# Performance work log

Measured on AMD Instinct MI355X. Metric: run time of the kernel, lower is better.

Reference implementation:

```python
import jax, jax.numpy as jnp
import numpy as np

N_KERNELS = 5
MUL_FACTOR = 2.0


def setup_inputs() -> dict:
    key = jax.random.key(0)
    k1, k2 = jax.random.split(key)
    X = jax.random.normal(k1, (4096, 512), dtype=jnp.float32)
    Y = jax.random.normal(k2, (4096, 512), dtype=jnp.float32)
    return {"X": X, "Y": Y}


def _mmd(X, Y):
    # multipliers: 2.0 ** (arange(5) - 2) = [0.25, 0.5, 1, 2, 4]
    mults = MUL_FACTOR ** (jnp.arange(N_KERNELS, dtype=jnp.float32) - N_KERNELS // 2)
    Z = jnp.concatenate([X, Y], axis=0)            # [N+M, D]
    n = Z.shape[0]
    # squared euclidean pairwise distances (cdist ** 2)
    sq = jnp.sum(Z * Z, axis=-1)                    # [N+M]
    D2 = sq[:, None] + sq[None, :] - 2.0 * (Z @ Z.T)
    D2 = jnp.maximum(D2, 0.0)                       # [N+M, N+M]
    # bandwidth from detached distances: sum / (n^2 - n)
    bw = jax.lax.stop_gradient(jnp.sum(D2)) / (n * n - n)
    # multi-bandwidth RBF sum over kernels
    K = jnp.sum(jnp.exp(-D2[None, :, :] / (bw * mults)[:, None, None]), axis=0)
    Nx = X.shape[0]
    XX = jnp.mean(K[:Nx, :Nx])
    XY = jnp.mean(K[:Nx, Nx:])
    YY = jnp.mean(K[Nx:, Nx:])
    return XX - 2.0 * XY + YY


def reference(X, Y):
    return _mmd(X, Y)
```

## Files before the change

kernel.cpp:

```cpp
#include <hip/hip_runtime.h>

#define N_ROWS 8192
#define NX     4096
#define DIM    512
#define BT     128
#define NT     64
#define BK     32

typedef __bf16 bf16_t;
typedef bf16_t bf16x8 __attribute__((ext_vector_type(8)));
typedef bf16_t bf16x4 __attribute__((ext_vector_type(4)));
typedef float  f32x4  __attribute__((ext_vector_type(4)));

#if __has_builtin(__builtin_amdgcn_exp2f)
  #define EXP2F __builtin_amdgcn_exp2f
#else
  #define EXP2F exp2f
#endif


__device__ __forceinline__ const float* zrow(const float* X, const float* Y, int r) {
    return (r < NX) ? (X + (size_t)r * DIM) : (Y + (size_t)(r - NX) * DIM);
}

__device__ __forceinline__ void gload_lds16(const bf16_t* g, bf16_t* l) {
    __builtin_amdgcn_global_load_lds(
        (__attribute__((address_space(1))) void*)(void*)(g),
        (__attribute__((address_space(3))) void*)(void*)(l), 16, 0, 0);
}

__global__ void k_prep(const float* __restrict__ X, const float* __restrict__ Y,
                       bf16_t* __restrict__ Zh, float* __restrict__ sqrow,
                       float* __restrict__ colsum) {
    int t = threadIdx.x;
    if (blockIdx.x == 0) { colsum[t] = 0.f; colsum[t + 256] = 0.f; }
    int wv = t >> 6, lane = t & 63;
    int row = blockIdx.x * 4 + wv;
    const float4* z4 = (const float4*)zrow(X, Y, row);
    float4 a = z4[lane], b = z4[lane + 64];
    bf16x4 ha = {(bf16_t)a.x, (bf16_t)a.y, (bf16_t)a.z, (bf16_t)a.w};
    bf16x4 hb = {(bf16_t)b.x, (bf16_t)b.y, (bf16_t)b.z, (bf16_t)b.w};
    *(bf16x4*)(Zh + (size_t)row * DIM + lane * 4) = ha;
    *(bf16x4*)(Zh + (size_t)row * DIM + 256 + lane * 4) = hb;
    float s = a.x*a.x + a.y*a.y + a.z*a.z + a.w*a.w
            + b.x*b.x + b.y*b.y + b.z*b.z + b.w*b.w;
    #pragma unroll
    for (int off = 32; off > 0; off >>= 1) s += __shfl_down(s, off);
    if (lane == 0) sqrow[row] = s;
}

__global__ void k_colsum(const float* X, const float* Y, float* colsum) {
    int c = threadIdx.x * 2;
    int r0 = blockIdx.x * 128;
    float s0 = 0.f, s1 = 0.f;
    for (int r = r0; r < r0 + 128; ++r) {
        const float* zr = zrow(X, Y, r);
        float2 v = *(const float2*)(zr + c);
        s0 += v.x; s1 += v.y;
    }
    atomicAdd(&colsum[c], s0);
    atomicAdd(&colsum[c + 1], s1);
}

__global__ void k_bw(const float* sqrow, const float* colsum, float* cvals, double* acc) {
    __shared__ double red[256];
    int t = threadIdx.x;
    double s1 = 0.0;
    for (int i = t; i < N_ROWS; i += 256) s1 += (double)sqrow[i];
    double cs = 0.0;
    for (int d = t; d < DIM; d += 256) { double v = colsum[d]; cs += v * v; }
    red[t] = s1; __syncthreads();
    for (int off = 128; off > 0; off >>= 1) { if (t < off) red[t] += red[t + off]; __syncthreads(); }
    double S1 = red[0]; __syncthreads();
    red[t] = cs; __syncthreads();
    for (int off = 128; off > 0; off >>= 1) { if (t < off) red[t] += red[t + off]; __syncthreads(); }
    if (t == 0) {
        double CS = red[0];
        double n = (double)N_ROWS;
        double sumD2 = 2.0 * n * S1 - 2.0 * CS;
        double bw = sumD2 / (n * n - n);
        const double LOG2E = 1.4426950408889634;
        double mult = 0.25;
        for (int k = 0; k < 5; ++k) {
            cvals[k] = (float)(-LOG2E / (bw * mult));
            mult *= 2.0;
        }
        *acc = 0.0;
    }
}

__global__ __launch_bounds__(256) void k_pair(const bf16_t* __restrict__ Zh,
                                              const float* __restrict__ sqrow,
                                              const float* __restrict__ cvals,
                                              double* acc) {
    int ti = blockIdx.x, tj = blockIdx.y;
    if (tj < ti) return;
    __shared__ bf16_t As[4096];
    __shared__ bf16_t Bs[4096];
    __shared__ float wsum[4];

    int t = threadIdx.x, lane = t & 63, wv = t >> 6;
    int wr = wv >> 1, wc = wv & 1;

    const bf16_t* gA[2]; const bf16_t* gB[2];
    bf16_t* ldsA[2]; bf16_t* ldsB[2];
    #pragma unroll
    for (int h = 0; h < 2; ++h) {
        int c = h * 256 + t;
        int r = c >> 2, sq = c & 3;
        int q = sq ^ ((r >> 1) & 3);
        gA[h] = Zh + (size_t)(ti * BT + r) * DIM + q * 8;
        gB[h] = Zh + (size_t)(tj * BT + r) * DIM + q * 8;
        int base = (h * 256 + wv * 64) * 8;
        ldsA[h] = As + base;
        ldsB[h] = Bs + base;
    }

    int n16 = lane & 15, q16 = lane >> 4;
    int aoff[4], boff[4];
    #pragma unroll
    for (int aa = 0; aa < 4; ++aa) {
        int r = 16 * (wr * 4 + aa) + n16;
        aoff[aa] = (r * 4 + (q16 ^ ((r >> 1) & 3))) * 8;
    }
    #pragma unroll
    for (int bb = 0; bb < 4; ++bb) {
        int r = 16 * (wc * 4 + bb) + n16;
        boff[bb] = (r * 4 + (q16 ^ ((r >> 1) & 3))) * 8;
    }

    f32x4 accf[4][4];
    #pragma unroll
    for (int a = 0; a < 4; ++a)
        #pragma unroll
        for (int b = 0; b < 4; ++b)
            accf[a][b] = (f32x4){0.f, 0.f, 0.f, 0.f};

    for (int kt = 0; kt < DIM; kt += BK) {
        if (kt) __syncthreads();
        #pragma unroll
        for (int h = 0; h < 2; ++h) {
            gload_lds16(gA[h] + kt, ldsA[h]);
            gload_lds16(gB[h] + kt, ldsB[h]);
        }
        __syncthreads();
        bf16x8 a[4], b[4];
        #pragma unroll
        for (int aa = 0; aa < 4; ++aa) a[aa] = *(const bf16x8*)(As + aoff[aa]);
        #pragma unroll
        for (int bb = 0; bb < 4; ++bb) b[bb] = *(const bf16x8*)(Bs + boff[bb]);
        #pragma unroll
        for (int aa = 0; aa < 4; ++aa)
            #pragma unroll
            for (int bb = 0; bb < 4; ++bb)
                accf[aa][bb] = __builtin_amdgcn_mfma_f32_16x16x32_bf16(
                    a[aa], b[bb], accf[aa][bb], 0, 0, 0);
    }

    float c4 = cvals[4];
    int i0 = ti * BT + wr * 64;
    int j0 = tj * BT + wc * 64;

    float sqi[4][4], sqj[4];
    #pragma unroll
    for (int aa = 0; aa < 4; ++aa)
        #pragma unroll
        for (int r = 0; r < 4; ++r)
            sqi[aa][r] = sqrow[i0 + 16 * aa + q16 * 4 + r];
    #pragma unroll
    for (int bb = 0; bb < 4; ++bb)
        sqj[bb] = sqrow[j0 + 16 * bb + n16];

    float s_local = 0.f;
    #pragma unroll
    for (int aa = 0; aa < 4; ++aa) {
        #pragma unroll
        for (int bb = 0; bb < 4; ++bb) {
            #pragma unroll
            for (int r = 0; r < 4; ++r) {
                float d2 = fmaf(-2.f, accf[aa][bb][r], sqi[aa][r] + sqj[bb]);
                d2 = fmaxf(d2, 0.f);
                float e4 = EXP2F(d2 * c4);
                float e3 = e4 * e4;
                float e2 = e3 * e3;
                float e1 = e2 * e2;
                float e0 = e1 * e1;
                s_local += e4 + e3 + e2 + e1 + e0;
            }
        }
    }
    #pragma unroll
    for (int off = 32; off > 0; off >>= 1) s_local += __shfl_down(s_local, off);
    if (lane == 0) wsum[wv] = s_local;
    __syncthreads();
    if (t == 0) {
        float bs = wsum[0] + wsum[1] + wsum[2] + wsum[3];
        double si = (ti < NT / 2) ? 1.0 : -1.0;
        double sj = (tj < NT / 2) ? 1.0 : -1.0;
        double w = si * sj * ((ti == tj) ? 1.0 : 2.0);
        atomicAdd(acc, w * (double)bs);
    }
}

__global__ void k_final(const double* acc, float* out) {
    out[0] = (float)(*acc / ((double)NX * (double)NX));
}

extern "C" void kernel_launch(void* const* d_in, const int* in_sizes, int n_in,
                              void* d_out, int out_size, void* d_ws, size_t ws_size,
                              hipStream_t stream) {
    const float* X = (const float*)d_in[0];
    const float* Y = (const float*)d_in[1];
    float* out = (float*)d_out;

    float*  sqrow  = (float*)d_ws;
    float*  colsum = sqrow + 8192;
    float*  cvals  = (float*)((char*)d_ws + 34816);
    double* acc    = (double*)((char*)d_ws + 34840);
    bf16_t* Zh     = (bf16_t*)((char*)d_ws + 36864);

    k_prep  <<<2048, 256, 0, stream>>>(X, Y, Zh, sqrow, colsum);
    k_colsum<<<64, 256, 0, stream>>>(X, Y, colsum);
    k_bw    <<<1, 256, 0, stream>>>(sqrow, colsum, cvals, acc);
    k_pair  <<<dim3(NT, NT), 256, 0, stream>>>(Zh, sqrow, cvals, acc);
    k_final <<<1, 1, 0, stream>>>(acc, out);
}
```

Baseline: 152.8 us.

## Pre-swizzle bf16 Z into MFMA fragment layout and drop LDS staging

The prep kernel now writes the bf16 copy of Z in an MFMA-fragment-ready layout, so the pair kernel loads its A/B operands straight from global memory into registers with a one-step prefetch. This removes the LDS staging and the per-k-step barriers. The column-sum kernel is merged into prep, and the final division moves into the pair kernel through a last-block counter, which saves two launches. The cost is that operand reuse now relies on L2/L1 caching instead of LDS sharing across waves, and extra register pressure comes from the prefetch buffers.

```diff
diff --git a/kernel.cpp b/kernel.cpp
--- a/kernel.cpp
+++ b/kernel.cpp
@@ -5,11 +5,12 @@
 #define DIM    512
 #define BT     128
 #define NT     64
-#define BK     32
+#define NB     (NT * (NT + 1) / 2)
+#define NGRP   512
+#define NCH    16
 
 typedef __bf16 bf16_t;
 typedef bf16_t bf16x8 __attribute__((ext_vector_type(8)));
-typedef bf16_t bf16x4 __attribute__((ext_vector_type(4)));
 typedef float  f32x4  __attribute__((ext_vector_type(4)));
 
 #if __has_builtin(__builtin_amdgcn_exp2f)
@@ -23,46 +24,50 @@
     return (r < NX) ? (X + (size_t)r * DIM) : (Y + (size_t)(r - NX) * DIM);
 }
 
-__device__ __forceinline__ void gload_lds16(const bf16_t* g, bf16_t* l) {
-    __builtin_amdgcn_global_load_lds(
-        (__attribute__((address_space(1))) void*)(void*)(g),
-        (__attribute__((address_space(3))) void*)(void*)(l), 16, 0, 0);
-}
-
 __global__ void k_prep(const float* __restrict__ X, const float* __restrict__ Y,
-                       bf16_t* __restrict__ Zh, float* __restrict__ sqrow,
+                       bf16_t* __restrict__ Zh2, float* __restrict__ sqrow,
                        float* __restrict__ colsum) {
     int t = threadIdx.x;
-    if (blockIdx.x == 0) { colsum[t] = 0.f; colsum[t + 256] = 0.f; }
-    int wv = t >> 6, lane = t & 63;
-    int row = blockIdx.x * 4 + wv;
-    const float4* z4 = (const float4*)zrow(X, Y, row);
-    float4 a = z4[lane], b = z4[lane + 64];
-    bf16x4 ha = {(bf16_t)a.x, (bf16_t)a.y, (bf16_t)a.z, (bf16_t)a.w};
-    bf16x4 hb = {(bf16_t)b.x, (bf16_t)b.y, (bf16_t)b.z, (bf16_t)b.w};
-    *(bf16x4*)(Zh + (size_t)row * DIM + lane * 4) = ha;
-    *(bf16x4*)(Zh + (size_t)row * DIM + 256 + lane * 4) = hb;
-    float s = a.x*a.x + a.y*a.y + a.z*a.z + a.w*a.w
-            + b.x*b.x + b.y*b.y + b.z*b.z + b.w*b.w;
-    #pragma unroll
-    for (int off = 32; off > 0; off >>= 1) s += __shfl_down(s, off);
-    if (lane == 0) sqrow[row] = s;
-}
-
-__global__ void k_colsum(const float* X, const float* Y, float* colsum) {
-    int c = threadIdx.x * 2;
-    int r0 = blockIdx.x * 128;
-    float s0 = 0.f, s1 = 0.f;
-    for (int r = r0; r < r0 + 128; ++r) {
-        const float* zr = zrow(X, Y, r);
-        float2 v = *(const float2*)(zr + c);
-        s0 += v.x; s1 += v.y;
-    }
-    atomicAdd(&colsum[c], s0);
-    atomicAdd(&colsum[c + 1], s1);
-}
-
-__global__ void k_bw(const float* sqrow, const float* colsum, float* cvals, double* acc) {
+    if (blockIdx.x < NGRP) {
+        int R = blockIdx.x;
+        __shared__ float lsq[16];
+        if (t < 16) lsq[t] = 0.f;
+        __syncthreads();
+        int C = t >> 4, u = t & 15;
+        int rbase = 4 * (u & 3);
+        int k = C * 32 + (u >> 2) * 8;
+        int l0 = (4 * t) & 63;
+        #pragma unroll
+        for (int i = 0; i < 4; ++i) {
+            int row = R * 16 + rbase + i;
+            const float* zr = zrow(X, Y, row) + k;
+            float4 va = *(const float4*)zr;
+            float4 vb = *(const float4*)(zr + 4);
+            bf16x8 h = {(bf16_t)va.x, (bf16_t)va.y, (bf16_t)va.z, (bf16_t)va.w,
+                        (bf16_t)vb.x, (bf16_t)vb.y, (bf16_t)vb.z, (bf16_t)vb.w};
+            *(bf16x8*)(Zh2 + ((size_t)(R * 16 + C) * 64 + (l0 + i)) * 8) = h;
+            float d = va.x*va.x + va.y*va.y + va.z*va.z + va.w*va.w
+                    + vb.x*vb.x + vb.y*vb.y + vb.z*vb.z + vb.w*vb.w;
+            atomicAdd(&lsq[rbase + i], d);
+        }
+        __syncthreads();
+        if (t < 16) sqrow[R * 16 + t] = lsq[t];
+    } else {
+        int b2 = blockIdx.x - NGRP;
+        int c = t * 2;
+        int r0 = b2 * 128;
+        float s0 = 0.f, s1 = 0.f;
+        for (int r = r0; r < r0 + 128; ++r) {
+            float2 v = *(const float2*)(zrow(X, Y, r) + c);
+            s0 += v.x; s1 += v.y;
+        }
+        atomicAdd(&colsum[c], s0);
+        atomicAdd(&colsum[c + 1], s1);
+    }
+}
+
+__global__ void k_bw(const float* __restrict__ sqrow, const float* __restrict__ colsum,
+                     float* cvals, double* acc, unsigned* done) {
     __shared__ double red[256];
     int t = threadIdx.x;
     double s1 = 0.0;
@@ -77,8 +82,7 @@
     if (t == 0) {
         double CS = red[0];
         double n = (double)N_ROWS;
-        double sumD2 = 2.0 * n * S1 - 2.0 * CS;
-        double bw = sumD2 / (n * n - n);
+        double bw = (2.0 * n * S1 - 2.0 * CS) / (n * n - n);
         const double LOG2E = 1.4426950408889634;
         double mult = 0.25;
         for (int k = 0; k < 5; ++k) {
@@ -86,48 +90,28 @@
             mult *= 2.0;
         }
         *acc = 0.0;
-    }
-}
-
-__global__ __launch_bounds__(256) void k_pair(const bf16_t* __restrict__ Zh,
+        *done = 0u;
+    }
+}
+
+__global__ __launch_bounds__(256) void k_pair(const bf16_t* __restrict__ Zh2,
                                               const float* __restrict__ sqrow,
                                               const float* __restrict__ cvals,
-                                              double* acc) {
+                                              double* acc, unsigned* done,
+                                              float* out) {
     int ti = blockIdx.x, tj = blockIdx.y;
     if (tj < ti) return;
-    __shared__ bf16_t As[4096];
-    __shared__ bf16_t Bs[4096];
-    __shared__ float wsum[4];
 
     int t = threadIdx.x, lane = t & 63, wv = t >> 6;
     int wr = wv >> 1, wc = wv & 1;
 
-    const bf16_t* gA[2]; const bf16_t* gB[2];
-    bf16_t* ldsA[2]; bf16_t* ldsB[2];
-    #pragma unroll
-    for (int h = 0; h < 2; ++h) {
-        int c = h * 256 + t;
-        int r = c >> 2, sq = c & 3;
-        int q = sq ^ ((r >> 1) & 3);
-        gA[h] = Zh + (size_t)(ti * BT + r) * DIM + q * 8;
-        gB[h] = Zh + (size_t)(tj * BT + r) * DIM + q * 8;
-        int base = (h * 256 + wv * 64) * 8;
-        ldsA[h] = As + base;
-        ldsB[h] = Bs + base;
-    }
-
-    int n16 = lane & 15, q16 = lane >> 4;
-    int aoff[4], boff[4];
-    #pragma unroll
-    for (int aa = 0; aa < 4; ++aa) {
-        int r = 16 * (wr * 4 + aa) + n16;
-        aoff[aa] = (r * 4 + (q16 ^ ((r >> 1) & 3))) * 8;
-    }
-    #pragma unroll
-    for (int bb = 0; bb < 4; ++bb) {
-        int r = 16 * (wc * 4 + bb) + n16;
-        boff[bb] = (r * 4 + (q16 ^ ((r >> 1) & 3))) * 8;
-    }
+    const bf16_t* pa[4]; const bf16_t* pb[4];
+    #pragma unroll
+    for (int aa = 0; aa < 4; ++aa)
+        pa[aa] = Zh2 + (size_t)(ti * 8 + wr * 4 + aa) * (16 * 512) + lane * 8;
+    #pragma unroll
+    for (int bb = 0; bb < 4; ++bb)
+        pb[bb] = Zh2 + (size_t)(tj * 8 + wc * 4 + bb) * (16 * 512) + lane * 8;
 
     f32x4 accf[4][4];
     #pragma unroll
@@ -136,28 +120,34 @@
         for (int b = 0; b < 4; ++b)
             accf[a][b] = (f32x4){0.f, 0.f, 0.f, 0.f};
 
-    for (int kt = 0; kt < DIM; kt += BK) {
-        if (kt) __syncthreads();
-        #pragma unroll
-        for (int h = 0; h < 2; ++h) {
-            gload_lds16(gA[h] + kt, ldsA[h]);
-            gload_lds16(gB[h] + kt, ldsB[h]);
-        }
-        __syncthreads();
-        bf16x8 a[4], b[4];
-        #pragma unroll
-        for (int aa = 0; aa < 4; ++aa) a[aa] = *(const bf16x8*)(As + aoff[aa]);
-        #pragma unroll
-        for (int bb = 0; bb < 4; ++bb) b[bb] = *(const bf16x8*)(Bs + boff[bb]);
+    bf16x8 a[4], b[4], an[4], bn[4];
+    #pragma unroll
+    for (int aa = 0; aa < 4; ++aa) a[aa] = *(const bf16x8*)(pa[aa]);
+    #pragma unroll
+    for (int bb = 0; bb < 4; ++bb) b[bb] = *(const bf16x8*)(pb[bb]);
+
+    #pragma unroll
+    for (int C = 0; C < NCH; ++C) {
+        if (C < NCH - 1) {
+            #pragma unroll
+            for (int aa = 0; aa < 4; ++aa) an[aa] = *(const bf16x8*)(pa[aa] + (C + 1) * 512);
+            #pragma unroll
+            for (int bb = 0; bb < 4; ++bb) bn[bb] = *(const bf16x8*)(pb[bb] + (C + 1) * 512);
+        }
         #pragma unroll
         for (int aa = 0; aa < 4; ++aa)
             #pragma unroll
             for (int bb = 0; bb < 4; ++bb)
                 accf[aa][bb] = __builtin_amdgcn_mfma_f32_16x16x32_bf16(
                     a[aa], b[bb], accf[aa][bb], 0, 0, 0);
+        #pragma unroll
+        for (int aa = 0; aa < 4; ++aa) a[aa] = an[aa];
+        #pragma unroll
+        for (int bb = 0; bb < 4; ++bb) b[bb] = bn[bb];
     }
 
     float c4 = cvals[4];
+    int n16 = lane & 15, q16 = lane >> 4;
     int i0 = ti * BT + wr * 64;
     int j0 = tj * BT + wc * 64;
 
@@ -191,6 +181,7 @@
     }
     #pragma unroll
     for (int off = 32; off > 0; off >>= 1) s_local += __shfl_down(s_local, off);
+    __shared__ float wsum[4];
     if (lane == 0) wsum[wv] = s_local;
     __syncthreads();
     if (t == 0) {
@@ -199,11 +190,14 @@
         double sj = (tj < NT / 2) ? 1.0 : -1.0;
         double w = si * sj * ((ti == tj) ? 1.0 : 2.0);
         atomicAdd(acc, w * (double)bs);
-    }
-}
-
-__global__ void k_final(const double* acc, float* out) {
-    out[0] = (float)(*acc / ((double)NX * (double)NX));
+        __threadfence();
+        unsigned old = atomicAdd(done, 1u);
+        if (old == NB - 1) {
+            __threadfence();
+            double tot = atomicAdd(acc, 0.0);
+            out[0] = (float)(tot / ((double)NX * (double)NX));
+        }
+    }
 }
 
 extern "C" void kernel_launch(void* const* d_in, const int* in_sizes, int n_in,
@@ -213,15 +207,15 @@
     const float* Y = (const float*)d_in[1];
     float* out = (float*)d_out;
 
-    float*  sqrow  = (float*)d_ws;
-    float*  colsum = sqrow + 8192;
-    float*  cvals  = (float*)((char*)d_ws + 34816);
-    double* acc    = (double*)((char*)d_ws + 34840);
-    bf16_t* Zh     = (bf16_t*)((char*)d_ws + 36864);
-
-    k_prep  <<<2048, 256, 0, stream>>>(X, Y, Zh, sqrow, colsum);
-    k_colsum<<<64, 256, 0, stream>>>(X, Y, colsum);
-    k_bw    <<<1, 256, 0, stream>>>(sqrow, colsum, cvals, acc);
-    k_pair  <<<dim3(NT, NT), 256, 0, stream>>>(Zh, sqrow, cvals, acc);
-    k_final <<<1, 1, 0, stream>>>(acc, out);
-}
+    float*    sqrow  = (float*)d_ws;
+    float*    colsum = (float*)((char*)d_ws + 32768);
+    float*    cvals  = (float*)((char*)d_ws + 34816);
+    double*   acc    = (double*)((char*)d_ws + 34848);
+    unsigned* done   = (unsigned*)((char*)d_ws + 34856);
+    bf16_t*   Zh2    = (bf16_t*)((char*)d_ws + 36864);
+
+    hipMemsetAsync(colsum, 0, 512 * sizeof(float), stream);
+    k_prep<<<NGRP + 64, 256, 0, stream>>>(X, Y, Zh2, sqrow, colsum);
+    k_bw  <<<1, 256, 0, stream>>>(sqrow, colsum, cvals, acc, done);
+    k_pair<<<dim3(NT, NT), 256, 0, stream>>>(Zh2, sqrow, cvals, acc, done, out);
+}
```

Result: slower. 234.6 us (+53.5%).

## Fuse all MMD stages into one persistent kernel with grid barriers

Applied to the files above, without the earlier changes.

Replaces the five separate launches with a single persistent kernel of 1280 blocks. The prep, column-sum and norm work are fused into one pass over the inputs. Software grid barriers separate the bandwidth computation from the pair stage, which walks only the upper-triangular tile list instead of launching and early-exiting the lower half. The final division is done by the last block through a completion counter. This removes launch gaps and redundant input reads, but adds spin-wait barriers that deadlock unless all 1280 blocks are co-resident, plus a memset before the launch.

```diff
diff --git a/kernel.cpp b/kernel.cpp
--- a/kernel.cpp
+++ b/kernel.cpp
@@ -5,11 +5,12 @@
 #define DIM    512
 #define BT     128
 #define NT     64
+#define NB     (NT * (NT + 1) / 2)
 #define BK     32
+#define GRID   1280
 
 typedef __bf16 bf16_t;
 typedef bf16_t bf16x8 __attribute__((ext_vector_type(8)));
-typedef bf16_t bf16x4 __attribute__((ext_vector_type(4)));
 typedef float  f32x4  __attribute__((ext_vector_type(4)));
 
 #if __has_builtin(__builtin_amdgcn_exp2f)
@@ -29,94 +30,98 @@
         (__attribute__((address_space(3))) void*)(void*)(l), 16, 0, 0);
 }
 
-__global__ void k_prep(const float* __restrict__ X, const float* __restrict__ Y,
-                       bf16_t* __restrict__ Zh, float* __restrict__ sqrow,
-                       float* __restrict__ colsum) {
-    int t = threadIdx.x;
-    if (blockIdx.x == 0) { colsum[t] = 0.f; colsum[t + 256] = 0.f; }
-    int wv = t >> 6, lane = t & 63;
-    int row = blockIdx.x * 4 + wv;
-    const float4* z4 = (const float4*)zrow(X, Y, row);
-    float4 a = z4[lane], b = z4[lane + 64];
-    bf16x4 ha = {(bf16_t)a.x, (bf16_t)a.y, (bf16_t)a.z, (bf16_t)a.w};
-    bf16x4 hb = {(bf16_t)b.x, (bf16_t)b.y, (bf16_t)b.z, (bf16_t)b.w};
-    *(bf16x4*)(Zh + (size_t)row * DIM + lane * 4) = ha;
-    *(bf16x4*)(Zh + (size_t)row * DIM + 256 + lane * 4) = hb;
-    float s = a.x*a.x + a.y*a.y + a.z*a.z + a.w*a.w
-            + b.x*b.x + b.y*b.y + b.z*b.z + b.w*b.w;
-    #pragma unroll
-    for (int off = 32; off > 0; off >>= 1) s += __shfl_down(s, off);
-    if (lane == 0) sqrow[row] = s;
-}
-
-__global__ void k_colsum(const float* X, const float* Y, float* colsum) {
-    int c = threadIdx.x * 2;
-    int r0 = blockIdx.x * 128;
-    float s0 = 0.f, s1 = 0.f;
-    for (int r = r0; r < r0 + 128; ++r) {
-        const float* zr = zrow(X, Y, r);
-        float2 v = *(const float2*)(zr + c);
-        s0 += v.x; s1 += v.y;
-    }
-    atomicAdd(&colsum[c], s0);
-    atomicAdd(&colsum[c + 1], s1);
-}
-
-__global__ void k_bw(const float* sqrow, const float* colsum, float* cvals, double* acc) {
-    __shared__ double red[256];
-    int t = threadIdx.x;
-    double s1 = 0.0;
-    for (int i = t; i < N_ROWS; i += 256) s1 += (double)sqrow[i];
-    double cs = 0.0;
-    for (int d = t; d < DIM; d += 256) { double v = colsum[d]; cs += v * v; }
-    red[t] = s1; __syncthreads();
-    for (int off = 128; off > 0; off >>= 1) { if (t < off) red[t] += red[t + off]; __syncthreads(); }
-    double S1 = red[0]; __syncthreads();
-    red[t] = cs; __syncthreads();
-    for (int off = 128; off > 0; off >>= 1) { if (t < off) red[t] += red[t + off]; __syncthreads(); }
-    if (t == 0) {
-        double CS = red[0];
-        double n = (double)N_ROWS;
-        double sumD2 = 2.0 * n * S1 - 2.0 * CS;
-        double bw = sumD2 / (n * n - n);
-        const double LOG2E = 1.4426950408889634;
-        double mult = 0.25;
-        for (int k = 0; k < 5; ++k) {
-            cvals[k] = (float)(-LOG2E / (bw * mult));
-            mult *= 2.0;
-        }
-        *acc = 0.0;
-    }
-}
-
-__global__ __launch_bounds__(256) void k_pair(const bf16_t* __restrict__ Zh,
-                                              const float* __restrict__ sqrow,
-                                              const float* __restrict__ cvals,
-                                              double* acc) {
-    int ti = blockIdx.x, tj = blockIdx.y;
-    if (tj < ti) return;
+__device__ __forceinline__ void gbar(unsigned* ctr) {
+    __syncthreads();
+    if (threadIdx.x == 0) {
+        __hip_atomic_fetch_add(ctr, 1u, __ATOMIC_ACQ_REL, __HIP_MEMORY_SCOPE_AGENT);
+        while (__hip_atomic_load(ctr, __ATOMIC_ACQUIRE, __HIP_MEMORY_SCOPE_AGENT) < (unsigned)GRID)
+            __builtin_amdgcn_s_sleep(2);
+    }
+    __syncthreads();
+}
+
+__global__ __launch_bounds__(256, 5) void k_all(const float* __restrict__ X,
+                                                const float* __restrict__ Y,
+                                                float* __restrict__ out,
+                                                char* __restrict__ ws) {
+    unsigned* ctr0   = (unsigned*)(ws + 0);
+    unsigned* ctr1   = (unsigned*)(ws + 4);
+    unsigned* done   = (unsigned*)(ws + 8);
+    double*   S1acc  = (double*)(ws + 16);
+    double*   acc    = (double*)(ws + 24);
+    float*    cvals  = (float*)(ws + 32);
+    float*    colsum = (float*)(ws + 64);
+    float*    sqrow  = (float*)(ws + 2176);
+    bf16_t*   Zh     = (bf16_t*)(ws + 36864);
+
     __shared__ bf16_t As[4096];
     __shared__ bf16_t Bs[4096];
     __shared__ float wsum[4];
 
     int t = threadIdx.x, lane = t & 63, wv = t >> 6;
+
+    if (blockIdx.x < 1024) {
+        float csum[8] = {0.f,0.f,0.f,0.f,0.f,0.f,0.f,0.f};
+        float s1part = 0.f;
+        float* cps = (float*)As;
+        #pragma unroll
+        for (int rp = 0; rp < 2; ++rp) {
+            int row = blockIdx.x * 8 + wv * 2 + rp;
+            const float* zr = zrow(X, Y, row) + lane * 8;
+            float4 a = *(const float4*)zr;
+            float4 c = *(const float4*)(zr + 4);
+            bf16x8 h = {(bf16_t)a.x, (bf16_t)a.y, (bf16_t)a.z, (bf16_t)a.w,
+                        (bf16_t)c.x, (bf16_t)c.y, (bf16_t)c.z, (bf16_t)c.w};
+            *(bf16x8*)(Zh + (size_t)row * DIM + lane * 8) = h;
+            csum[0] += a.x; csum[1] += a.y; csum[2] += a.z; csum[3] += a.w;
+            csum[4] += c.x; csum[5] += c.y; csum[6] += c.z; csum[7] += c.w;
+            float s = a.x*a.x + a.y*a.y + a.z*a.z + a.w*a.w
+                    + c.x*c.x + c.y*c.y + c.z*c.z + c.w*c.w;
+            #pragma unroll
+            for (int off = 32; off > 0; off >>= 1) s += __shfl_down(s, off);
+            if (lane == 0) { sqrow[row] = s; s1part += s; }
+        }
+        #pragma unroll
+        for (int j = 0; j < 8; ++j) cps[wv * 512 + lane * 8 + j] = csum[j];
+        if (lane == 0) wsum[wv] = s1part;
+        __syncthreads();
+        #pragma unroll
+        for (int cc = 0; cc < 2; ++cc) {
+            int c = t * 2 + cc;
+            float tot = cps[c] + cps[512 + c] + cps[1024 + c] + cps[1536 + c];
+            atomicAdd(&colsum[c], tot);
+        }
+        if (t == 0) atomicAdd(S1acc, (double)(wsum[0] + wsum[1] + wsum[2] + wsum[3]));
+    }
+    gbar(ctr0);
+
+    if (blockIdx.x == 0) {
+        double cs = 0.0;
+        for (int c = t; c < 512; c += 256) { double v = colsum[c]; cs += v * v; }
+        double* red = (double*)As;
+        red[t] = cs; __syncthreads();
+        for (int off = 128; off > 0; off >>= 1) {
+            if (t < off) red[t] += red[t + off];
+            __syncthreads();
+        }
+        if (t == 0) {
+            double S1 = *S1acc;
+            double n = (double)N_ROWS;
+            double bw = (2.0 * n * S1 - 2.0 * red[0]) / (n * n - n);
+            const double LOG2E = 1.4426950408889634;
+            double mult = 0.25;
+            for (int k = 0; k < 5; ++k) {
+                cvals[k] = (float)(-LOG2E / (bw * mult));
+                mult *= 2.0;
+            }
+        }
+    }
+    gbar(ctr1);
+
+    float c4 = cvals[4];
+    int n16 = lane & 15, q16 = lane >> 4;
     int wr = wv >> 1, wc = wv & 1;
 
-    const bf16_t* gA[2]; const bf16_t* gB[2];
-    bf16_t* ldsA[2]; bf16_t* ldsB[2];
-    #pragma unroll
-    for (int h = 0; h < 2; ++h) {
-        int c = h * 256 + t;
-        int r = c >> 2, sq = c & 3;
-        int q = sq ^ ((r >> 1) & 3);
-        gA[h] = Zh + (size_t)(ti * BT + r) * DIM + q * 8;
-        gB[h] = Zh + (size_t)(tj * BT + r) * DIM + q * 8;
-        int base = (h * 256 + wv * 64) * 8;
-        ldsA[h] = As + base;
-        ldsB[h] = Bs + base;
-    }
-
-    int n16 = lane & 15, q16 = lane >> 4;
     int aoff[4], boff[4];
     #pragma unroll
     for (int aa = 0; aa < 4; ++aa) {
@@ -128,82 +133,99 @@
         int r = 16 * (wc * 4 + bb) + n16;
         boff[bb] = (r * 4 + (q16 ^ ((r >> 1) & 3))) * 8;
     }
-
-    f32x4 accf[4][4];
-    #pragma unroll
-    for (int a = 0; a < 4; ++a)
-        #pragma unroll
-        for (int b = 0; b < 4; ++b)
-            accf[a][b] = (f32x4){0.f, 0.f, 0.f, 0.f};
-
-    for (int kt = 0; kt < DIM; kt += BK) {
-        if (kt) __syncthreads();
-        #pragma unroll
-        for (int h = 0; h < 2; ++h) {
-            gload_lds16(gA[h] + kt, ldsA[h]);
-            gload_lds16(gB[h] + kt, ldsB[h]);
-        }
+    int c0_ = t, c1_ = t + 256;
+    int r0_ = c0_ >> 2, q0_ = (c0_ & 3) ^ ((r0_ >> 1) & 3);
+    int r1_ = c1_ >> 2, q1_ = (c1_ & 3) ^ ((r1_ >> 1) & 3);
+    int ldsoff0 = (0 * 256 + wv * 64) * 8;
+    int ldsoff1 = (1 * 256 + wv * 64) * 8;
+
+    for (int idx = blockIdx.x; idx < NB; idx += GRID) {
+        int tj = (int)((sqrtf(8.f * (float)idx + 1.f) - 1.f) * 0.5f);
+        while ((tj + 1) * (tj + 2) / 2 <= idx) ++tj;
+        while (tj * (tj + 1) / 2 > idx) --tj;
+        int ti = idx - tj * (tj + 1) / 2;
+
+        const bf16_t* gA0 = Zh + (size_t)(ti * BT + r0_) * DIM + q0_ * 8;
+        const bf16_t* gA1 = Zh + (size_t)(ti * BT + r1_) * DIM + q1_ * 8;
+        const bf16_t* gB0 = Zh + (size_t)(tj * BT + r0_) * DIM + q0_ * 8;
+        const bf16_t* gB1 = Zh + (size_t)(tj * BT + r1_) * DIM + q1_ * 8;
+
+        f32x4 accf[4][4];
+        #pragma unroll
+        for (int a = 0; a < 4; ++a)
+            #pragma unroll
+            for (int b = 0; b < 4; ++b)
+                accf[a][b] = (f32x4){0.f, 0.f, 0.f, 0.f};
+
+        for (int kt = 0; kt < DIM; kt += BK) {
+            if (kt) __syncthreads();
+            gload_lds16(gA0 + kt, As + ldsoff0);
+            gload_lds16(gA1 + kt, As + ldsoff1);
+            gload_lds16(gB0 + kt, Bs + ldsoff0);
+            gload_lds16(gB1 + kt, Bs + ldsoff1);
+            __syncthreads();
+            bf16x8 a[4], b[4];
+            #pragma unroll
+            for (int aa = 0; aa < 4; ++aa) a[aa] = *(const bf16x8*)(As + aoff[aa]);
+            #pragma unroll
+            for (int bb = 0; bb < 4; ++bb) b[bb] = *(const bf16x8*)(Bs + boff[bb]);
+            #pragma unroll
+            for (int aa = 0; aa < 4; ++aa)
+                #pragma unroll
+                for (int bb = 0; bb < 4; ++bb)
+                    accf[aa][bb] = __builtin_amdgcn_mfma_f32_16x16x32_bf16(
+                        a[aa], b[bb], accf[aa][bb], 0, 0, 0);
+        }
+
+        int i0 = ti * BT + wr * 64;
+        int j0 = tj * BT + wc * 64;
+        float sqi[4][4], sqj[4];
+        #pragma unroll
+        for (int aa = 0; aa < 4; ++aa)
+            #pragma unroll
+            for (int r = 0; r < 4; ++r)
+                sqi[aa][r] = sqrow[i0 + 16 * aa + q16 * 4 + r];
+        #pragma unroll
+        for (int bb = 0; bb < 4; ++bb)
+            sqj[bb] = sqrow[j0 + 16 * bb + n16];
+
+        float s_local = 0.f;
+        #pragma unroll
+        for (int aa = 0; aa < 4; ++aa) {
+            #pragma unroll
+            for (int bb = 0; bb < 4; ++bb) {
+                #pragma unroll
+                for (int r = 0; r < 4; ++r) {
+                    float d2 = fmaf(-2.f, accf[aa][bb][r], sqi[aa][r] + sqj[bb]);
+                    d2 = fmaxf(d2, 0.f);
+                    float e4 = EXP2F(d2 * c4);
+                    float e3 = e4 * e4;
+                    float e2 = e3 * e3;
+                    float e1 = e2 * e2;
+                    float e0 = e1 * e1;
+                    s_local += e4 + e3 + e2 + e1 + e0;
+                }
+            }
+        }
+        #pragma unroll
+        for (int off = 32; off > 0; off >>= 1) s_local += __shfl_down(s_local, off);
+        if (lane == 0) wsum[wv] = s_local;
         __syncthreads();
-        bf16x8 a[4], b[4];
-        #pragma unroll
-        for (int aa = 0; aa < 4; ++aa) a[aa] = *(const bf16x8*)(As + aoff[aa]);
-        #pragma unroll
-        for (int bb = 0; bb < 4; ++bb) b[bb] = *(const bf16x8*)(Bs + boff[bb]);
-        #pragma unroll
-        for (int aa = 0; aa < 4; ++aa)
-            #pragma unroll
-            for (int bb = 0; bb < 4; ++bb)
-                accf[aa][bb] = __builtin_amdgcn_mfma_f32_16x16x32_bf16(
-                    a[aa], b[bb], accf[aa][bb], 0, 0, 0);
-    }
-
-    float c4 = cvals[4];
-    int i0 = ti * BT + wr * 64;
-    int j0 = tj * BT + wc * 64;
-
-    float sqi[4][4], sqj[4];
-    #pragma unroll
-    for (int aa = 0; aa < 4; ++aa)
-        #pragma unroll
-        for (int r = 0; r < 4; ++r)
-            sqi[aa][r] = sqrow[i0 + 16 * aa + q16 * 4 + r];
-    #pragma unroll
-    for (int bb = 0; bb < 4; ++bb)
-        sqj[bb] = sqrow[j0 + 16 * bb + n16];
-
-    float s_local = 0.f;
-    #pragma unroll
-    for (int aa = 0; aa < 4; ++aa) {
-        #pragma unroll
-        for (int bb = 0; bb < 4; ++bb) {
-            #pragma unroll
-            for (int r = 0; r < 4; ++r) {
-                float d2 = fmaf(-2.f, accf[aa][bb][r], sqi[aa][r] + sqj[bb]);
-                d2 = fmaxf(d2, 0.f);
-                float e4 = EXP2F(d2 * c4);
-                float e3 = e4 * e4;
-                float e2 = e3 * e3;
-                float e1 = e2 * e2;
-                float e0 = e1 * e1;
-                s_local += e4 + e3 + e2 + e1 + e0;
+        if (t == 0) {
+            float bs = wsum[0] + wsum[1] + wsum[2] + wsum[3];
+            double si = (ti < NT / 2) ? 1.0 : -1.0;
+            double sj = (tj < NT / 2) ? 1.0 : -1.0;
+            double w = si * sj * ((ti == tj) ? 1.0 : 2.0);
+            atomicAdd(acc, w * (double)bs);
+            __threadfence();
+            unsigned old = atomicAdd(done, 1u);
+            if (old == NB - 1) {
+                __threadfence();
+                double tot = atomicAdd(acc, 0.0);
+                out[0] = (float)(tot / ((double)NX * (double)NX));
             }
         }
     }
-    #pragma unroll
-    for (int off = 32; off > 0; off >>= 1) s_local += __shfl_down(s_local, off);
-    if (lane == 0) wsum[wv] = s_local;
-    __syncthreads();
-    if (t == 0) {
-        float bs = wsum[0] + wsum[1] + wsum[2] + wsum[3];
-        double si = (ti < NT / 2) ? 1.0 : -1.0;
-        double sj = (tj < NT / 2) ? 1.0 : -1.0;
-        double w = si * sj * ((ti == tj) ? 1.0 : 2.0);
-        atomicAdd(acc, w * (double)bs);
-    }
-}
-
-__global__ void k_final(const double* acc, float* out) {
-    out[0] = (float)(*acc / ((double)NX * (double)NX));
 }
 
 extern "C" void kernel_launch(void* const* d_in, const int* in_sizes, int n_in,
@@ -213,15 +235,6 @@
     const float* Y = (const float*)d_in[1];
     float* out = (float*)d_out;
 
-    float*  sqrow  = (float*)d_ws;
-    float*  colsum = sqrow + 8192;
-    float*  cvals  = (float*)((char*)d_ws + 34816);
-    double* acc    = (double*)((char*)d_ws + 34840);
-    bf16_t* Zh     = (bf16_t*)((char*)d_ws + 36864);
-
-    k_prep  <<<2048, 256, 0, stream>>>(X, Y, Zh, sqrow, colsum);
-    k_colsum<<<64, 256, 0, stream>>>(X, Y, colsum);
-    k_bw    <<<1, 256, 0, stream>>>(sqrow, colsum, cvals, acc);
-    k_pair  <<<dim3(NT, NT), 256, 0, stream>>>(Zh, sqrow, cvals, acc);
-    k_final <<<1, 1, 0, stream>>>(acc, out);
-}
+    hipMemsetAsync(d_ws, 0, 2112, stream);
+    k_all<<<GRID, 256, 0, stream>>>(X, Y, out, (char*)d_ws);
+}
```

Measured after the change: 440.1 us. 188% more time.
